# Optimization experiments

Hardware: AMD Instinct MI355X
Metric: run time of the kernel (lower is better)

The kernel has to match this reference:

```python
import jax, jax.numpy as jnp
import numpy as np
import math

B, S, E, H, DFF = 8, 1024, 1024, 16, 4096
DK = E // H
EPS = 1e-6


def _layernorm(x, alpha, bias):
    # Faithful to the torch module: uses unbiased std (ddof=1) and divides by (std + eps)
    mean = jnp.mean(x, axis=-1, keepdims=True)
    var = jnp.sum((x - mean) ** 2, axis=-1, keepdims=True) / (x.shape[-1] - 1)
    std = jnp.sqrt(var)
    return alpha * (x - mean) / (std + EPS) + bias


def setup_inputs() -> dict:
    key = jax.random.key(0)
    ks = jax.random.split(key, 16)
    sc_e = 1.0 / math.sqrt(E)
    sc_f = 1.0 / math.sqrt(DFF)
    inp = {
        "x": jax.random.normal(ks[0], (B, S, E), dtype=jnp.float32),
        "mask": jnp.ones((1, 1, S, S), dtype=jnp.int32),
        # linear weights stored as (in, out)
        "wq": jax.random.normal(ks[1], (E, E), jnp.float32) * sc_e,
        "bq": jnp.zeros((E,), jnp.float32),
        "wk": jax.random.normal(ks[2], (E, E), jnp.float32) * sc_e,
        "bk": jnp.zeros((E,), jnp.float32),
        "wv": jax.random.normal(ks[3], (E, E), jnp.float32) * sc_e,
        "bv": jnp.zeros((E,), jnp.float32),
        "wo": jax.random.normal(ks[4], (E, E), jnp.float32) * sc_e,
        "bo": jnp.zeros((E,), jnp.float32),
        "w1": jax.random.normal(ks[5], (E, DFF), jnp.float32) * sc_e,
        "b1": jnp.zeros((DFF,), jnp.float32),
        "w2": jax.random.normal(ks[6], (DFF, E), jnp.float32) * sc_f,
        "b2": jnp.zeros((E,), jnp.float32),
        "ln1_a": jnp.ones((E,), jnp.float32),
        "ln1_b": jnp.zeros((E,), jnp.float32),
        "ln2_a": jnp.ones((E,), jnp.float32),
        "ln2_b": jnp.zeros((E,), jnp.float32),
    }
    return inp


def _mha(x, mask, wq, bq, wk, bk, wv, bv, wo, bo):
    q = (x @ wq + bq).reshape(B, S, H, DK).transpose(0, 2, 1, 3)  # [B,H,S,DK]
    k = (x @ wk + bk).reshape(B, S, H, DK).transpose(0, 2, 1, 3)
    v = (x @ wv + bv).reshape(B, S, H, DK).transpose(0, 2, 1, 3)
    scores = jnp.einsum("bhqd,bhkd->bhqk", q, k) / math.sqrt(DK)  # [B,H,S,S]
    scores = jnp.where(mask == 0, jnp.float32(-1e9), scores)
    attn = jax.nn.softmax(scores, axis=-1)
    out = jnp.einsum("bhqk,bhkd->bhqd", attn, v)  # [B,H,S,DK]
    out = out.transpose(0, 2, 1, 3).reshape(B, S, E)
    return out @ wo + bo


def reference(x, mask, wq, bq, wk, bk, wv, bv, wo, bo, w1, b1, w2, b2,
              ln1_a, ln1_b, ln2_a, ln2_b):
    # Residual connection 1 (pre-norm): x + dropout(attn(norm(x))) ; dropout=0 at eval
    h1 = x + _mha(_layernorm(x, ln1_a, ln1_b), mask, wq, bq, wk, bk, wv, bv, wo, bo)
    # Residual connection 2: h1 + ffn(norm(h1))
    n2 = _layernorm(h1, ln2_a, ln2_b)
    ff = jax.nn.relu(n2 @ w1 + b1) @ w2 + b2
    return h1 + ff
```

## Files before the change

kernel.cpp:

```cpp
#include <hip/hip_runtime.h>
#include <hip/hip_bf16.h>
#include <cstdint>
#include <cstddef>

#define BB   8
#define SS   1024
#define EE   1024
#define HH   16
#define DKK  64
#define DFFN 4096
#define NROWS (BB*SS)

typedef __attribute__((ext_vector_type(8))) short short8;
typedef __attribute__((ext_vector_type(4))) short s16x4;
typedef __attribute__((ext_vector_type(4))) float f32x4;

__device__ __forceinline__ short f2bf(float f) {
  __hip_bfloat16 h = __float2bfloat16(f);
  return __builtin_bit_cast(short, h);
}

__device__ __forceinline__ void gload_lds16(const void* g, void* l) {
  __builtin_amdgcn_global_load_lds((const __attribute__((address_space(1))) void*)g,
                                   (__attribute__((address_space(3))) void*)l, 16, 0, 0);
}

__device__ __forceinline__ f32x4 mfma16(s16x4 a, s16x4 b, f32x4 c) {
#if __has_builtin(__builtin_amdgcn_mfma_f32_16x16x16_bf16)
  return __builtin_amdgcn_mfma_f32_16x16x16_bf16(a, b, c, 0, 0, 0);
#elif __has_builtin(__builtin_amdgcn_mfma_f32_16x16x16bf16_1k)
  return __builtin_amdgcn_mfma_f32_16x16x16bf16_1k(a, b, c, 0, 0, 0);
#else
  f32x4 d = c;
  asm("v_mfma_f32_16x16x16_bf16 %0, %1, %2, %0" : "+v"(d) : "v"(a), "v"(b));
  return d;
#endif
}

__global__ __launch_bounds__(256) void wtrans_kernel(const float* __restrict__ in,
                                                     short* __restrict__ out,
                                                     int R, int C) {
  __shared__ float tile[32][33];
  int c0 = blockIdx.x * 32, r0 = blockIdx.y * 32;
  int tx = threadIdx.x, ty = threadIdx.y;
#pragma unroll
  for (int i = 0; i < 32; i += 8)
    tile[ty + i][tx] = in[(size_t)(r0 + ty + i) * C + (c0 + tx)];
  __syncthreads();
#pragma unroll
  for (int i = 0; i < 32; i += 8)
    out[(size_t)(c0 + ty + i) * R + (r0 + tx)] = f2bf(tile[tx][ty + i]);
}

__global__ __launch_bounds__(256) void ln_kernel(const float* __restrict__ x,
                                                 const float* __restrict__ alpha,
                                                 const float* __restrict__ beta,
                                                 short* __restrict__ out) {
  __shared__ float sbuf[4];
  int row = blockIdx.x;
  int tid = threadIdx.x;
  const float* xr = x + (size_t)row * EE;
  float4 v = reinterpret_cast<const float4*>(xr)[tid];
  float s = v.x + v.y + v.z + v.w;
#pragma unroll
  for (int o = 32; o > 0; o >>= 1) s += __shfl_down(s, o);
  if ((tid & 63) == 0) sbuf[tid >> 6] = s;
  __syncthreads();
  float mean = (sbuf[0] + sbuf[1] + sbuf[2] + sbuf[3]) * (1.0f / EE);
  __syncthreads();
  float dx = v.x - mean, dy = v.y - mean, dz = v.z - mean, dw = v.w - mean;
  float sq = dx * dx + dy * dy + dz * dz + dw * dw;
#pragma unroll
  for (int o = 32; o > 0; o >>= 1) sq += __shfl_down(sq, o);
  if ((tid & 63) == 0) sbuf[tid >> 6] = sq;
  __syncthreads();
  float var = (sbuf[0] + sbuf[1] + sbuf[2] + sbuf[3]) * (1.0f / (EE - 1));
  float inv = 1.0f / (sqrtf(var) + 1e-6f);
  float4 a = reinterpret_cast<const float4*>(alpha)[tid];
  float4 b = reinterpret_cast<const float4*>(beta)[tid];
  size_t base = (size_t)row * EE + tid * 4;
  out[base + 0] = f2bf(a.x * dx * inv + b.x);
  out[base + 1] = f2bf(a.y * dy * inv + b.y);
  out[base + 2] = f2bf(a.z * dz * inv + b.z);
  out[base + 3] = f2bf(a.w * dw * inv + b.w);
}

template <int EPI>
__global__ __launch_bounds__(512, 2) void gemm256(const short* __restrict__ A,
                                                  const short* __restrict__ Bt,
                                                  const float* __restrict__ bias,
                                                  const float* __restrict__ resid,
                                                  void* __restrict__ out,
                                                  int N, int K, int NTN) {
  extern __shared__ char lds[];
  int tid = threadIdx.x, lane = tid & 63, w = tid >> 6;
  int wm = w >> 2, wn = w & 3;
  int g = lane >> 4, c = lane & 15;

  int nwg = gridDim.x, wg = blockIdx.x;
  int swg = (wg & 7) * (nwg >> 3) + (wg >> 3);
  int mt = swg / NTN, nt = swg % NTN;
  int m0 = mt * 256, n0 = nt * 256;

  int rS = tid >> 3;
  int gslot = (tid & 7) ^ ((tid >> 4) & 7);
  const short* pA = A + (size_t)(m0 + rS) * K + gslot * 8;
  const short* pB = Bt + (size_t)(n0 + rS) * K + gslot * 8;

#define STAGE_A(b, h, T)                                                                   \
  {                                                                                        \
    gload_lds16(pA + (size_t)((h)*128) * K + (size_t)(T)*64,                               \
                lds + (b)*32768 + (h)*16384 + tid * 16);                                   \
    gload_lds16(pA + (size_t)((h)*128 + 64) * K + (size_t)(T)*64,                          \
                lds + (b)*32768 + (h)*16384 + 8192 + tid * 16);                            \
  }
#define STAGE_B(b, h, T)                                                                   \
  {                                                                                        \
    gload_lds16(pB + (size_t)((h)*128) * K + (size_t)(T)*64,                               \
                lds + 65536 + (b)*32768 + (h)*16384 + tid * 16);                           \
    gload_lds16(pB + (size_t)((h)*128 + 64) * K + (size_t)(T)*64,                          \
                lds + 65536 + (b)*32768 + (h)*16384 + 8192 + tid * 16);                    \
  }
#define WAITV(NN) asm volatile("s_waitcnt vmcnt(" #NN ")" ::: "memory")

  int aoff0 = ((0 * 4 + g) ^ (c >> 1)) * 16;
  int aoff1 = ((1 * 4 + g) ^ (c >> 1)) * 16;
  char* ldsAb = lds + (wm * 128 + c) * 128;
  char* ldsBb = lds + 65536 + (wn * 64 + c) * 128;

  f32x4 acc[8][4] = {};
  short8 af[2][2], bfr[4][2];

#define READB(b)                                                                           \
  {                                                                                        \
    _Pragma("unroll") for (int nf = 0; nf < 4; ++nf) {                                     \
      bfr[nf][0] = *(const short8*)(ldsBb + (b)*32768 + nf * 2048 + aoff0);                \
      bfr[nf][1] = *(const short8*)(ldsBb + (b)*32768 + nf * 2048 + aoff1);                \
    }                                                                                      \
  }

#define PHASE(b, q, STAGEOP, ENDWAIT)                                                      \
  {                                                                                        \
    _Pragma("unroll") for (int mi = 0; mi < 2; ++mi) {                                     \
      af[mi][0] = *(const short8*)(ldsAb + (b)*32768 + ((q)*32 + mi * 16) * 128 + aoff0);  \
      af[mi][1] = *(const short8*)(ldsAb + (b)*32768 + ((q)*32 + mi * 16) * 128 + aoff1);  \
    }                                                                                      \
    STAGEOP;                                                                               \
    __builtin_amdgcn_s_barrier();                                                          \
    asm volatile("s_waitcnt lgkmcnt(0)" ::: "memory");                                     \
    __builtin_amdgcn_sched_barrier(0);                                                     \
    __builtin_amdgcn_s_setprio(1);                                                         \
    _Pragma("unroll") for (int mi = 0; mi < 2; ++mi)                                       \
      _Pragma("unroll") for (int nf = 0; nf < 4; ++nf) {                                   \
        acc[(q)*2 + mi][nf] = __builtin_amdgcn_mfma_f32_16x16x32_bf16(                     \
            af[mi][0], bfr[nf][0], acc[(q)*2 + mi][nf], 0, 0, 0);                          \
        acc[(q)*2 + mi][nf] = __builtin_amdgcn_mfma_f32_16x16x32_bf16(                     \
            af[mi][1], bfr[nf][1], acc[(q)*2 + mi][nf], 0, 0, 0);                          \
      }                                                                                    \
    __builtin_amdgcn_s_setprio(0);                                                         \
    ENDWAIT;                                                                               \
    __builtin_amdgcn_s_barrier();                                                          \
  }

  int NKT = K >> 6;

  STAGE_A(0, 0, 0); STAGE_A(0, 1, 0);
  STAGE_B(0, 0, 0); STAGE_B(0, 1, 0);
  STAGE_B(1, 0, 1); STAGE_B(1, 1, 1);
  WAITV(4);
  __builtin_amdgcn_s_barrier();

  for (int t = 0; t < NKT - 2; t += 2) {
    READB(0);
    PHASE(0, 0, STAGE_A(1, 0, t + 1), );
    PHASE(0, 1, STAGE_A(1, 1, t + 1), );
    PHASE(0, 2, STAGE_B(0, 0, t + 2), );
    PHASE(0, 3, STAGE_B(0, 1, t + 2), WAITV(4));
    READB(1);
    PHASE(1, 0, STAGE_A(0, 0, t + 2), );
    PHASE(1, 1, STAGE_A(0, 1, t + 2), );
    PHASE(1, 2, STAGE_B(1, 0, t + 3), );
    PHASE(1, 3, STAGE_B(1, 1, t + 3), WAITV(4));
  }
  {
    int t = NKT - 2;
    READB(0);
    PHASE(0, 0, STAGE_A(1, 0, t + 1), );
    PHASE(0, 1, STAGE_A(1, 1, t + 1), );
    PHASE(0, 2, , );
    PHASE(0, 3, , WAITV(0));
    READB(1);
    PHASE(1, 0, , );
    PHASE(1, 1, , );
    PHASE(1, 2, , );
    PHASE(1, 3, , );
  }

#undef STAGE_A
#undef STAGE_B
#undef READB
#undef PHASE
#undef WAITV

  int rb_ = m0 + wm * 128;
  int cb_ = n0 + wn * 64;
#pragma unroll
  for (int fm = 0; fm < 8; ++fm) {
#pragma unroll
    for (int nf = 0; nf < 4; ++nf) {
      int col = cb_ + nf * 16 + c;
      float bv = bias[col];
      if (EPI == 5) {
        int which = col >> 10;
        int inner = col & 1023;
        int h = inner >> 6, d = inner & 63;
        if (which < 2) {
          short* dst = (short*)out + (size_t)which * (8u * 1024 * 1024);
#pragma unroll
          for (int j = 0; j < 4; ++j) {
            int row = rb_ + fm * 16 + g * 4 + j;
            int b = row >> 10, s = row & 1023;
            dst[(((size_t)(b * HH + h)) * SS + s) * DKK + d] = f2bf(acc[fm][nf][j] + bv);
          }
        } else {
          int row0 = rb_ + fm * 16 + g * 4;
          int b = row0 >> 10, s0 = row0 & 1023;
          s16x4 pkv;
#pragma unroll
          for (int j = 0; j < 4; ++j) pkv[j] = f2bf(acc[fm][nf][j] + bv);
          *(s16x4*)((short*)out + 2u * 8 * 1024 * 1024 +
                    (((size_t)(b * HH + h)) * DKK + d) * SS + s0) = pkv;
        }
      } else {
#pragma unroll
        for (int j = 0; j < 4; ++j) {
          int row = rb_ + fm * 16 + g * 4 + j;
          float val = acc[fm][nf][j] + bv;
          if (EPI == 1) {
            ((short*)out)[(size_t)row * N + col] = f2bf(val > 0.f ? val : 0.f);
          } else {
            ((float*)out)[(size_t)row * N + col] = resid[(size_t)row * N + col] + val;
          }
        }
      }
    }
  }
}

template <int EPI>
__global__ __launch_bounds__(256, 4) void gemm_bt(const short* __restrict__ A,
                                                  const short* __restrict__ Bt,
                                                  const float* __restrict__ bias,
                                                  const float* __restrict__ resid,
                                                  void* __restrict__ out,
                                                  int N, int K, int NTN) {
  __shared__ short As[2][4096];
  __shared__ short Bs[2][4096];
  int tid = threadIdx.x;
  int lane = tid & 63, w = tid >> 6;
  int wr = w >> 1, wc = w & 1;
  int g = lane >> 4, c = lane & 15;

  int nwg = gridDim.x;
  int wg = blockIdx.x;
  int swg = (wg & 7) * (nwg >> 3) + (wg >> 3);
  int mt = swg / NTN, nt = swg % NTN;
  int m0 = mt * 128, n0 = nt * 128;

  int r0 = tid >> 2;
  int gslot = (tid & 3) ^ ((r0 >> 1) & 3);
  const short* pA = A + (size_t)(m0 + r0) * K + gslot * 8;
  const short* pB = Bt + (size_t)(n0 + r0) * K + gslot * 8;
  const size_t row64 = (size_t)64 * K;

  f32x4 acc[4][4] = {};

#define STAGE(B, T)                                                             \
  {                                                                             \
    gload_lds16(pA + (size_t)(T) * 32,         (char*)As[B] + w * 1024);        \
    gload_lds16(pA + (size_t)(T) * 32 + row64, (char*)As[B] + 4096 + w * 1024); \
    gload_lds16(pB + (size_t)(T) * 32,         (char*)Bs[B] + w * 1024);        \
    gload_lds16(pB + (size_t)(T) * 32 + row64, (char*)Bs[B] + 4096 + w * 1024); \
  }

  int NKT = K >> 5;
  STAGE(0, 0);
  __syncthreads();
  int buf = 0;

  int so = (g ^ ((c >> 1) & 3)) * 8;

  for (int t = 0; t < NKT; ++t) {
    if (t + 1 < NKT) STAGE(buf ^ 1, t + 1);

    short8 af[4], bfr[4];
#pragma unroll
    for (int i = 0; i < 4; ++i) {
      af[i]  = *(const short8*)&As[buf][(wr * 64 + i * 16 + c) * 32 + so];
      bfr[i] = *(const short8*)&Bs[buf][(wc * 64 + i * 16 + c) * 32 + so];
    }
    __builtin_amdgcn_s_setprio(1);
#pragma unroll
    for (int mi = 0; mi < 4; ++mi)
#pragma unroll
      for (int nf = 0; nf < 4; ++nf)
        acc[mi][nf] = __builtin_amdgcn_mfma_f32_16x16x32_bf16(af[mi], bfr[nf], acc[mi][nf], 0, 0, 0);
    __builtin_amdgcn_s_setprio(0);
    __syncthreads();
    buf ^= 1;
  }
#undef STAGE

  int rb_ = m0 + wr * 64;
  int cb_ = n0 + wc * 64;
#pragma unroll
  for (int mi = 0; mi < 4; ++mi) {
#pragma unroll
    for (int nf = 0; nf < 4; ++nf) {
      int col = cb_ + nf * 16 + c;
      float bv = bias[col];
#pragma unroll
      for (int j = 0; j < 4; ++j) {
        int row = rb_ + mi * 16 + g * 4 + j;
        float val = acc[mi][nf][j] + bv;
        if (EPI == 1) {
          ((short*)out)[(size_t)row * N + col] = f2bf(val > 0.f ? val : 0.f);
        } else {
          ((float*)out)[(size_t)row * N + col] = resid[(size_t)row * N + col] + val;
        }
      }
    }
  }
}

__global__ __launch_bounds__(256, 3) void attn_kernel(const short* __restrict__ q,
                                                      const short* __restrict__ k,
                                                      const short* __restrict__ vt,
                                                      short* __restrict__ out) {
  __shared__ short Ks[2][64 * 64];
  __shared__ short Vs[2][64 * 64];
  int bh = blockIdx.x, qt = blockIdx.y;
  int tid = threadIdx.x, lane = tid & 63, w = tid >> 6;
  int g = lane >> 4, c = lane & 15;
  const short* qp = q + (size_t)bh * SS * DKK;
  const short* kp = k + (size_t)bh * SS * DKK;
  const short* vp = vt + (size_t)bh * DKK * SS;

  int q0 = qt * 128 + w * 32;

  short8 qf[2][2];
#pragma unroll
  for (int qb = 0; qb < 2; ++qb)
#pragma unroll
    for (int ks = 0; ks < 2; ++ks)
      qf[qb][ks] = *(const short8*)(qp + (size_t)(q0 + qb * 16 + c) * DKK + ks * 32 + g * 8);

  f32x4 oacc[2][4];
#pragma unroll
  for (int qb = 0; qb < 2; ++qb)
#pragma unroll
    for (int nd = 0; nd < 4; ++nd)
#pragma unroll
      for (int j = 0; j < 4; ++j) oacc[qb][nd][j] = 0.f;
  float mrun[2] = {-1e30f, -1e30f}, lrun[2] = {0.f, 0.f};

  int rs = lane >> 3;
  int cs = lane & 7;
  int swz = (cs ^ rs) * 8;

  int buf = 0;
#define STAGE(B, T)                                                                  \
  {                                                                                  \
    _Pragma("unroll")                                                                \
    for (int cc = 0; cc < 2; ++cc) {                                                 \
      int chunk = w * 2 + cc;                                                        \
      int row = chunk * 8 + rs;                                                      \
      gload_lds16(kp + (size_t)((T) * 64 + row) * DKK + swz, &Ks[B][chunk * 512]);   \
      gload_lds16(vp + (size_t)row * SS + (T) * 64 + swz, &Vs[B][chunk * 512]);      \
    }                                                                                \
  }

  STAGE(0, 0);
  __syncthreads();

  for (int t = 0; t < SS / 64; ++t) {
    if (t < SS / 64 - 1) STAGE(buf ^ 1, t + 1);

    f32x4 sc[2][4];
#pragma unroll
    for (int qb = 0; qb < 2; ++qb)
#pragma unroll
      for (int nf = 0; nf < 4; ++nf)
#pragma unroll
        for (int j = 0; j < 4; ++j) sc[qb][nf][j] = 0.f;
#pragma unroll
    for (int ks = 0; ks < 2; ++ks) {
      short8 kf[4];
#pragma unroll
      for (int nf = 0; nf < 4; ++nf) {
        int row = nf * 16 + c;
        int off = row * 64 + (((ks * 64 + g * 16) ^ ((c & 7) << 4)) >> 1);
        kf[nf] = *(const short8*)&Ks[buf][off];
      }
#pragma unroll
      for (int qb = 0; qb < 2; ++qb)
#pragma unroll
        for (int nf = 0; nf < 4; ++nf)
          sc[qb][nf] = __builtin_amdgcn_mfma_f32_16x16x32_bf16(kf[nf], qf[qb][ks], sc[qb][nf], 0, 0, 0);
    }

    s16x4 pk[2][4];
    float corr[2];
#pragma unroll
    for (int qb = 0; qb < 2; ++qb) {
      float pm = -1e30f;
#pragma unroll
      for (int nf = 0; nf < 4; ++nf)
#pragma unroll
        for (int j = 0; j < 4; ++j) pm = fmaxf(pm, sc[qb][nf][j]);
      pm = fmaxf(pm, __shfl_xor(pm, 16));
      pm = fmaxf(pm, __shfl_xor(pm, 32));
      pm *= 0.125f;
      float mnew = fmaxf(mrun[qb], pm);
      corr[qb] = __expf(mrun[qb] - mnew);
      mrun[qb] = mnew;
      float rsum = 0.f;
#pragma unroll
      for (int nf = 0; nf < 4; ++nf) {
        float p0 = __expf(sc[qb][nf][0] * 0.125f - mnew);
        float p1 = __expf(sc[qb][nf][1] * 0.125f - mnew);
        float p2 = __expf(sc[qb][nf][2] * 0.125f - mnew);
        float p3 = __expf(sc[qb][nf][3] * 0.125f - mnew);
        rsum += (p0 + p1) + (p2 + p3);
        pk[qb][nf][0] = f2bf(p0); pk[qb][nf][1] = f2bf(p1);
        pk[qb][nf][2] = f2bf(p2); pk[qb][nf][3] = f2bf(p3);
      }
      rsum += __shfl_xor(rsum, 16);
      rsum += __shfl_xor(rsum, 32);
      lrun[qb] = lrun[qb] * corr[qb] + rsum;
    }
#pragma unroll
    for (int qb = 0; qb < 2; ++qb) {
      float cj[4];
#pragma unroll
      for (int j = 0; j < 4; ++j) cj[j] = __shfl(corr[qb], (lane & 48) | (g * 4 + j));
#pragma unroll
      for (int nd = 0; nd < 4; ++nd)
#pragma unroll
        for (int j = 0; j < 4; ++j) oacc[qb][nd][j] *= cj[j];
    }

#pragma unroll
    for (int nf = 0; nf < 4; ++nf) {
      s16x4 vf[4];
#pragma unroll
      for (int nd = 0; nd < 4; ++nd) {
        int row = nd * 16 + c;
        int off = row * 64 + (((nf * 32 + g * 8) ^ ((c & 7) << 4)) >> 1);
        vf[nd] = *(const s16x4*)&Vs[buf][off];
      }
#pragma unroll
      for (int qb = 0; qb < 2; ++qb)
#pragma unroll
        for (int nd = 0; nd < 4; ++nd)
          oacc[qb][nd] = mfma16(pk[qb][nf], vf[nd], oacc[qb][nd]);
    }
    __syncthreads();
    buf ^= 1;
  }
#undef STAGE

  int b = bh >> 4, h = bh & 15;
#pragma unroll
  for (int qb = 0; qb < 2; ++qb) {
#pragma unroll
    for (int j = 0; j < 4; ++j) {
      float linv = 1.0f / __shfl(lrun[qb], (lane & 48) | (g * 4 + j));
      int srow = q0 + qb * 16 + g * 4 + j;
#pragma unroll
      for (int nd = 0; nd < 4; ++nd)
        out[((size_t)b * SS + srow) * EE + h * DKK + nd * 16 + c] = f2bf(oacc[qb][nd][j] * linv);
    }
  }
}

extern "C" void kernel_launch(void* const* d_in, const int* in_sizes, int n_in,
                              void* d_out, int out_size, void* d_ws, size_t ws_size,
                              hipStream_t stream) {
  (void)in_sizes; (void)n_in; (void)out_size; (void)ws_size;
  const float* x   = (const float*)d_in[0];
  const float* wq  = (const float*)d_in[2];  const float* bq  = (const float*)d_in[3];
  const float* wk  = (const float*)d_in[4];  const float* bk  = (const float*)d_in[5];
  const float* wv  = (const float*)d_in[6];  const float* bv  = (const float*)d_in[7];
  const float* wo  = (const float*)d_in[8];  const float* bo  = (const float*)d_in[9];
  const float* w1  = (const float*)d_in[10]; const float* b1  = (const float*)d_in[11];
  const float* w2  = (const float*)d_in[12]; const float* b2  = (const float*)d_in[13];
  const float* l1a = (const float*)d_in[14]; const float* l1b = (const float*)d_in[15];
  const float* l2a = (const float*)d_in[16]; const float* l2b = (const float*)d_in[17];
  float* out = (float*)d_out;

  char* ws = (char*)d_ws;
  const size_t MB = 1024ull * 1024ull;
  short* wqkvT = (short*)(ws + 0 * MB);
  short* woT = (short*)(ws + 6 * MB);
  short* w1T = (short*)(ws + 8 * MB);
  short* w2T = (short*)(ws + 16 * MB);
  short* n1  = (short*)(ws + 24 * MB);
  short* qb  = (short*)(ws + 40 * MB);
  short* ff1 = (short*)(ws + 40 * MB);
  short* ao  = (short*)(ws + 88 * MB);
  float* bqkv = (float*)(ws + 100 * MB);
  float* h1  = (float*)(ws + 104 * MB);

  hipMemcpyAsync(bqkv,        bq, EE * sizeof(float), hipMemcpyDeviceToDevice, stream);
  hipMemcpyAsync(bqkv + EE,   bk, EE * sizeof(float), hipMemcpyDeviceToDevice, stream);
  hipMemcpyAsync(bqkv + 2*EE, bv, EE * sizeof(float), hipMemcpyDeviceToDevice, stream);

  dim3 tb(32, 8);
  wtrans_kernel<<<dim3(EE / 32, EE / 32), tb, 0, stream>>>(wq, wqkvT, EE, EE);
  wtrans_kernel<<<dim3(EE / 32, EE / 32), tb, 0, stream>>>(wk, wqkvT + 1024 * 1024, EE, EE);
  wtrans_kernel<<<dim3(EE / 32, EE / 32), tb, 0, stream>>>(wv, wqkvT + 2 * 1024 * 1024, EE, EE);
  wtrans_kernel<<<dim3(EE / 32, EE / 32), tb, 0, stream>>>(wo, woT, EE, EE);
  wtrans_kernel<<<dim3(DFFN / 32, EE / 32), tb, 0, stream>>>(w1, w1T, EE, DFFN);
  wtrans_kernel<<<dim3(EE / 32, DFFN / 32), tb, 0, stream>>>(w2, w2T, DFFN, EE);

  ln_kernel<<<NROWS, 256, 0, stream>>>(x, l1a, l1b, n1);

  gemm256<5><<<dim3(32 * 12), 512, 131072, stream>>>(n1, wqkvT, bqkv, nullptr, qb, 3072, EE, 12);

  attn_kernel<<<dim3(BB * HH, SS / 128), 256, 0, stream>>>(qb, qb + 8 * 1024 * 1024,
                                                           qb + 16 * 1024 * 1024, ao);

  gemm_bt<2><<<dim3(64 * 8), 256, 0, stream>>>(ao, woT, bo, x, h1, EE, EE, 8);

  ln_kernel<<<NROWS, 256, 0, stream>>>(h1, l2a, l2b, n1);

  gemm256<1><<<dim3(32 * 16), 512, 131072, stream>>>(n1, w1T, b1, nullptr, ff1, DFFN, EE, 16);
  gemm_bt<2><<<dim3(64 * 8), 256, 0, stream>>>(ff1, w2T, b2, h1, out, EE, DFFN, 8);
}
```

Measured before the change: 385.2 us.

## Replace 128x128 gemm_bt with 256x128 ping-pong pipelined GEMM for N=1024 projections

Swaps the small 128x128 tile, K=32-step GEMM used for the output projection and the FFN down-projection for a 512-thread kernel with a 256x128 tile and a K=64 step. It double-buffers A and B in 96KB of dynamic LDS, splits each k-step into phases that interleave the next stage's global-to-LDS loads with MFMA work, and uses explicit waitcnt and barriers. The aim is better operand reuse and fewer barriers per FLOP. In exchange the grid shrinks to 256 workgroups at one block per CU, which lowers occupancy and may leave CUs idle or imbalanced.

```diff
diff --git a/kernel.cpp b/kernel.cpp
--- a/kernel.cpp
+++ b/kernel.cpp
@@ -247,87 +247,122 @@
   }
 }
 
-template <int EPI>
-__global__ __launch_bounds__(256, 4) void gemm_bt(const short* __restrict__ A,
-                                                  const short* __restrict__ Bt,
-                                                  const float* __restrict__ bias,
-                                                  const float* __restrict__ resid,
-                                                  void* __restrict__ out,
-                                                  int N, int K, int NTN) {
-  __shared__ short As[2][4096];
-  __shared__ short Bs[2][4096];
-  int tid = threadIdx.x;
-  int lane = tid & 63, w = tid >> 6;
-  int wr = w >> 1, wc = w & 1;
+__global__ __launch_bounds__(512, 1) void gemm256x128(const short* __restrict__ A,
+                                                      const short* __restrict__ Bt,
+                                                      const float* __restrict__ bias,
+                                                      const float* __restrict__ resid,
+                                                      float* __restrict__ out,
+                                                      int N, int K, int NTN) {
+  extern __shared__ char lds[];
+  int tid = threadIdx.x, lane = tid & 63, w = tid >> 6;
+  int wm = w >> 1, wn = w & 1;
   int g = lane >> 4, c = lane & 15;
 
-  int nwg = gridDim.x;
-  int wg = blockIdx.x;
+  int nwg = gridDim.x, wg = blockIdx.x;
   int swg = (wg & 7) * (nwg >> 3) + (wg >> 3);
   int mt = swg / NTN, nt = swg % NTN;
-  int m0 = mt * 128, n0 = nt * 128;
-
-  int r0 = tid >> 2;
-  int gslot = (tid & 3) ^ ((r0 >> 1) & 3);
-  const short* pA = A + (size_t)(m0 + r0) * K + gslot * 8;
-  const short* pB = Bt + (size_t)(n0 + r0) * K + gslot * 8;
-  const size_t row64 = (size_t)64 * K;
+  int m0 = mt * 256, n0 = nt * 128;
+
+  int rS = tid >> 3;
+  int gslot = (tid & 7) ^ ((tid >> 4) & 7);
+  const short* pA = A + (size_t)(m0 + rS) * K + gslot * 8;
+  const short* pB = Bt + (size_t)(n0 + rS) * K + gslot * 8;
+
+#define STAGE_A(b, h, T)                                                                   \
+  {                                                                                        \
+    gload_lds16(pA + (size_t)((h)*128) * K + (size_t)(T)*64,                               \
+                lds + (b)*32768 + (h)*16384 + tid * 16);                                   \
+    gload_lds16(pA + (size_t)((h)*128 + 64) * K + (size_t)(T)*64,                          \
+                lds + (b)*32768 + (h)*16384 + 8192 + tid * 16);                            \
+  }
+#define STAGE_B(b, T)                                                                      \
+  {                                                                                        \
+    gload_lds16(pB + (size_t)(T)*64,            lds + 65536 + (b)*16384 + tid * 16);       \
+    gload_lds16(pB + (size_t)64 * K + (size_t)(T)*64,                                      \
+                lds + 65536 + (b)*16384 + 8192 + tid * 16);                                \
+  }
+#define WAITV(NN) asm volatile("s_waitcnt vmcnt(" #NN ")" ::: "memory")
+
+  int aoff0 = ((0 * 4 + g) ^ (c >> 1)) * 16;
+  int aoff1 = ((1 * 4 + g) ^ (c >> 1)) * 16;
+  char* ldsAb = lds + (wm * 64 + c) * 128;
+  char* ldsBb = lds + 65536 + (wn * 64 + c) * 128;
 
   f32x4 acc[4][4] = {};
-
-#define STAGE(B, T)                                                             \
-  {                                                                             \
-    gload_lds16(pA + (size_t)(T) * 32,         (char*)As[B] + w * 1024);        \
-    gload_lds16(pA + (size_t)(T) * 32 + row64, (char*)As[B] + 4096 + w * 1024); \
-    gload_lds16(pB + (size_t)(T) * 32,         (char*)Bs[B] + w * 1024);        \
-    gload_lds16(pB + (size_t)(T) * 32 + row64, (char*)Bs[B] + 4096 + w * 1024); \
-  }
-
-  int NKT = K >> 5;
-  STAGE(0, 0);
-  __syncthreads();
-  int buf = 0;
-
-  int so = (g ^ ((c >> 1) & 3)) * 8;
-
-  for (int t = 0; t < NKT; ++t) {
-    if (t + 1 < NKT) STAGE(buf ^ 1, t + 1);
-
-    short8 af[4], bfr[4];
-#pragma unroll
-    for (int i = 0; i < 4; ++i) {
-      af[i]  = *(const short8*)&As[buf][(wr * 64 + i * 16 + c) * 32 + so];
-      bfr[i] = *(const short8*)&Bs[buf][(wc * 64 + i * 16 + c) * 32 + so];
-    }
-    __builtin_amdgcn_s_setprio(1);
-#pragma unroll
-    for (int mi = 0; mi < 4; ++mi)
-#pragma unroll
-      for (int nf = 0; nf < 4; ++nf)
-        acc[mi][nf] = __builtin_amdgcn_mfma_f32_16x16x32_bf16(af[mi], bfr[nf], acc[mi][nf], 0, 0, 0);
-    __builtin_amdgcn_s_setprio(0);
-    __syncthreads();
-    buf ^= 1;
-  }
-#undef STAGE
-
-  int rb_ = m0 + wr * 64;
-  int cb_ = n0 + wc * 64;
-#pragma unroll
-  for (int mi = 0; mi < 4; ++mi) {
+  short8 af[2][2], bfr[4][2];
+
+#define READB(b)                                                                           \
+  {                                                                                        \
+    _Pragma("unroll") for (int nf = 0; nf < 4; ++nf) {                                     \
+      bfr[nf][0] = *(const short8*)(ldsBb + (b)*16384 + nf * 2048 + aoff0);                \
+      bfr[nf][1] = *(const short8*)(ldsBb + (b)*16384 + nf * 2048 + aoff1);                \
+    }                                                                                      \
+  }
+
+#define PHASE(b, q, STAGEOP, ENDWAIT)                                                      \
+  {                                                                                        \
+    _Pragma("unroll") for (int mi = 0; mi < 2; ++mi) {                                     \
+      af[mi][0] = *(const short8*)(ldsAb + (b)*32768 + ((q)*32 + mi * 16) * 128 + aoff0);  \
+      af[mi][1] = *(const short8*)(ldsAb + (b)*32768 + ((q)*32 + mi * 16) * 128 + aoff1);  \
+    }                                                                                      \
+    STAGEOP;                                                                               \
+    __builtin_amdgcn_s_barrier();                                                          \
+    asm volatile("s_waitcnt lgkmcnt(0)" ::: "memory");                                     \
+    __builtin_amdgcn_sched_barrier(0);                                                     \
+    __builtin_amdgcn_s_setprio(1);                                                         \
+    _Pragma("unroll") for (int mi = 0; mi < 2; ++mi)                                       \
+      _Pragma("unroll") for (int nf = 0; nf < 4; ++nf) {                                   \
+        acc[(q)*2 + mi][nf] = __builtin_amdgcn_mfma_f32_16x16x32_bf16(                     \
+            af[mi][0], bfr[nf][0], acc[(q)*2 + mi][nf], 0, 0, 0);                          \
+        acc[(q)*2 + mi][nf] = __builtin_amdgcn_mfma_f32_16x16x32_bf16(                     \
+            af[mi][1], bfr[nf][1], acc[(q)*2 + mi][nf], 0, 0, 0);                          \
+      }                                                                                    \
+    __builtin_amdgcn_s_setprio(0);                                                         \
+    ENDWAIT;                                                                               \
+    __builtin_amdgcn_s_barrier();                                                          \
+  }
+
+  int NKT = K >> 6;
+
+  STAGE_A(0, 0, 0); STAGE_A(0, 1, 0);
+  STAGE_B(0, 0);
+  STAGE_B(1, 1);
+  WAITV(2);
+  __builtin_amdgcn_s_barrier();
+
+  for (int t = 0; t < NKT - 2; t += 2) {
+    READB(0);
+    PHASE(0, 0, STAGE_A(1, 0, t + 1); STAGE_A(1, 1, t + 1), );
+    PHASE(0, 1, STAGE_B(0, t + 2), WAITV(2));
+    READB(1);
+    PHASE(1, 0, STAGE_A(0, 0, t + 2); STAGE_A(0, 1, t + 2), );
+    PHASE(1, 1, STAGE_B(1, t + 3), WAITV(2));
+  }
+  READB(0);
+  PHASE(0, 0, STAGE_A(1, 0, NKT - 1); STAGE_A(1, 1, NKT - 1), );
+  PHASE(0, 1, , WAITV(0));
+  READB(1);
+  PHASE(1, 0, , );
+  PHASE(1, 1, , );
+
+#undef STAGE_A
+#undef STAGE_B
+#undef READB
+#undef PHASE
+#undef WAITV
+
+  int rb_ = m0 + wm * 64;
+  int cb_ = n0 + wn * 64;
+#pragma unroll
+  for (int fm = 0; fm < 4; ++fm) {
 #pragma unroll
     for (int nf = 0; nf < 4; ++nf) {
       int col = cb_ + nf * 16 + c;
       float bv = bias[col];
 #pragma unroll
       for (int j = 0; j < 4; ++j) {
-        int row = rb_ + mi * 16 + g * 4 + j;
-        float val = acc[mi][nf][j] + bv;
-        if (EPI == 1) {
-          ((short*)out)[(size_t)row * N + col] = f2bf(val > 0.f ? val : 0.f);
-        } else {
-          ((float*)out)[(size_t)row * N + col] = resid[(size_t)row * N + col] + val;
-        }
+        int row = rb_ + fm * 16 + g * 4 + j;
+        out[(size_t)row * N + col] = resid[(size_t)row * N + col] + acc[fm][nf][j] + bv;
       }
     }
   }
@@ -531,10 +566,10 @@
   attn_kernel<<<dim3(BB * HH, SS / 128), 256, 0, stream>>>(qb, qb + 8 * 1024 * 1024,
                                                            qb + 16 * 1024 * 1024, ao);
 
-  gemm_bt<2><<<dim3(64 * 8), 256, 0, stream>>>(ao, woT, bo, x, h1, EE, EE, 8);
+  gemm256x128<<<dim3(256), 512, 98304, stream>>>(ao, woT, bo, x, h1, EE, EE, 8);
 
   ln_kernel<<<NROWS, 256, 0, stream>>>(h1, l2a, l2b, n1);
 
   gemm256<1><<<dim3(32 * 16), 512, 131072, stream>>>(n1, w1T, b1, nullptr, ff1, DFFN, EE, 16);
-  gemm_bt<2><<<dim3(64 * 8), 256, 0, stream>>>(ff1, w2T, b2, h1, out, EE, DFFN, 8);
-}
+  gemm256x128<<<dim3(256), 512, 98304, stream>>>(ff1, w2T, b2, h1, out, EE, DFFN, 8);
+}
```

After: 374.3 us. 1.03x faster.
